# Kernel tuning notes

Measured on AMD Instinct MI355X. Metric: run time of the kernel, lower is better.

The kernel has to match this reference:

```python
import jax, jax.numpy as jnp
import numpy as np

FEAT = 1152
HID = [768, 512, 256]
WS = 32
LN_EPS = 1e-5


def _ln(x, g, b):
    mu = jnp.mean(x, axis=-1, keepdims=True)
    var = jnp.mean(jnp.square(x - mu), axis=-1, keepdims=True)
    return (x - mu) * jax.lax.rsqrt(var + LN_EPS) * g + b


def setup_inputs() -> dict:
    key = jax.random.key(0)
    ks = jax.random.split(key, 16)
    B, N, C = 8, 9216, FEAT

    def lin(k, din, dout):
        s = 1.0 / np.sqrt(din)
        k1, k2 = jax.random.split(k)
        return (jax.random.uniform(k1, (din, dout), jnp.float32, -s, s),
                jax.random.uniform(k2, (dout,), jnp.float32, -s, s))

    x = jax.random.normal(ks[0], (B, N, C), jnp.float32)
    W1, b1 = lin(ks[1], C, HID[0])
    W2, b2 = lin(ks[2], HID[0], HID[1])
    W3, b3 = lin(ks[3], HID[1], HID[2])
    Wo, bo = lin(ks[4], HID[2], C)
    red = C // 8
    ca_w1, ca_b1 = lin(ks[5], C, red)
    ca_w2, ca_b2 = lin(ks[6], red, C)
    return {
        "x": x,
        "W1": W1, "b1": b1, "g1": jnp.ones((HID[0],)), "be1": jnp.zeros((HID[0],)),
        "W2": W2, "b2": b2, "g2": jnp.ones((HID[1],)), "be2": jnp.zeros((HID[1],)),
        "W3": W3, "b3": b3, "g3": jnp.ones((HID[2],)), "be3": jnp.zeros((HID[2],)),
        "Wo": Wo, "bo": bo,
        "ca_w1": ca_w1, "ca_b1": ca_b1, "ca_w2": ca_w2, "ca_b2": ca_b2,
    }


def reference(x, W1, b1, g1, be1, W2, b2, g2, be2, W3, b3, g3, be3,
              Wo, bo, ca_w1, ca_b1, ca_w2, ca_b2):
    B, N, C = x.shape
    # projection + hidden blocks: Linear -> GELU(exact) -> LayerNorm
    h = _ln(jax.nn.gelu(x @ W1 + b1, approximate=False), g1, be1)
    h = _ln(jax.nn.gelu(h @ W2 + b2, approximate=False), g2, be2)
    h = _ln(jax.nn.gelu(h @ W3 + b3, approximate=False), g3, be3)
    y = h @ Wo + bo  # (B, N, C)
    # SE channel attention: global avg-pool over seq, 1x1 convs (=linear)
    pooled = jnp.mean(y, axis=1)                                  # (B, C)
    s = jax.nn.relu(pooled @ ca_w1 + ca_b1)                       # (B, C/8)
    s = jax.nn.sigmoid(s @ ca_w2 + ca_b2)                         # (B, C)
    y = y * s[:, None, :]
    # block-diagonal local self-attention, window = WS, scale 1/sqrt(C)
    nw = N // WS
    yw = y.reshape(B, nw, WS, C)
    scores = jnp.einsum('bwqc,bwkc->bwqk', yw, yw) / jnp.sqrt(jnp.asarray(C, y.dtype))
    attn = jax.nn.softmax(scores, axis=-1)
    out = jnp.einsum('bwqk,bwkc->bwqc', attn, yw)
    return out.reshape(B, N, C)
```

## Files before the change

kernel.cpp:

```cpp
#include <hip/hip_runtime.h>
#include <cstdint>
#include <cstddef>

typedef __bf16 bf16;
typedef __bf16 bf16x8 __attribute__((ext_vector_type(8)));
typedef float f32x4 __attribute__((ext_vector_type(4)));

__device__ __forceinline__ void gload_lds16(const bf16* g, bf16* l) {
    __builtin_amdgcn_global_load_lds((const __attribute__((address_space(1))) void*)g,
                                     (__attribute__((address_space(3))) void*)l, 16, 0, 0);
}

__global__ void wtrans_kernel(const float* __restrict__ W, bf16* __restrict__ Wt, int K, int N) {
    __shared__ bf16 tile[64][65];
    const int t = threadIdx.x;
    const int k0 = blockIdx.x << 6;
    const int n0 = blockIdx.y << 6;
#pragma unroll
    for (int i = 0; i < 16; ++i) {
        const int flat = i * 256 + t;
        const int r = flat >> 6;
        const int c = flat & 63;
        tile[c][r] = (bf16)W[(size_t)(k0 + r) * N + n0 + c];
    }
    __syncthreads();
#pragma unroll
    for (int i = 0; i < 16; ++i) {
        const int flat = i * 256 + t;
        const int r = flat >> 6;
        const int c = flat & 63;
        Wt[(size_t)(n0 + r) * K + k0 + c] = tile[r][c];
    }
}

__device__ __forceinline__ int xcd_swz(int bid, int nwg) {
    return (bid & 7) * (nwg >> 3) + (bid >> 3);
}

__global__ void gemm_bf16_kernel(const bf16* __restrict__ A, const bf16* __restrict__ Bt,
                                 const float* __restrict__ bias, bf16* __restrict__ C,
                                 int K, int N, int nx, int do_gelu)
{
    __shared__ bf16 Alds[128 * 64];
    __shared__ bf16 Blds[128 * 64];
    const int t = threadIdx.x;
    const int w = t >> 6;
    const int l = t & 63;
    const int l15 = l & 15, l4 = l >> 4;
    const int wgid = xcd_swz(blockIdx.x, gridDim.x);
    const int mblk = wgid / nx;
    const int nblk = wgid - mblk * nx;
    const int m0 = mblk << 7;
    const int n0 = nblk << 7;
    const int wm = (w >> 1) << 6;
    const int wn = (w & 1) << 6;

    f32x4 acc[4][4] = {};

    int sr[4], sg[4];
#pragma unroll
    for (int i = 0; i < 4; ++i) {
        const int flat = i * 256 + t;
        sr[i] = flat >> 3;
        sg[i] = ((flat & 7) ^ (sr[i] & 7)) << 3;
    }

    for (int k0 = 0; k0 < K; k0 += 64) {
#pragma unroll
        for (int i = 0; i < 4; ++i) {
            gload_lds16(A + (size_t)(m0 + sr[i]) * K + (k0 + sg[i]),
                        &Alds[(size_t)(i * 256 + (w << 6)) << 3]);
            gload_lds16(Bt + (size_t)(n0 + sr[i]) * K + (k0 + sg[i]),
                        &Blds[(size_t)(i * 256 + (w << 6)) << 3]);
        }
        __syncthreads();
#pragma unroll
        for (int kk = 0; kk < 2; ++kk) {
            bf16x8 af[4], bfv[4];
#pragma unroll
            for (int i = 0; i < 4; ++i) {
                const int r = wm + (i << 4) + l15;
                const int g = (kk << 2) + l4;
                af[i] = *(const bf16x8*)&Alds[(r << 6) + ((g ^ (r & 7)) << 3)];
                const int rn = wn + (i << 4) + l15;
                bfv[i] = *(const bf16x8*)&Blds[(rn << 6) + ((g ^ (rn & 7)) << 3)];
            }
#pragma unroll
            for (int i = 0; i < 4; ++i)
#pragma unroll
                for (int j = 0; j < 4; ++j)
                    acc[i][j] = __builtin_amdgcn_mfma_f32_16x16x32_bf16(af[i], bfv[j], acc[i][j], 0, 0, 0);
        }
        __syncthreads();
    }

#pragma unroll
    for (int i = 0; i < 4; ++i) {
        const int mb = m0 + wm + (i << 4) + (l4 << 2);
#pragma unroll
        for (int j = 0; j < 4; ++j) {
            const int col = n0 + wn + (j << 4) + l15;
            const float bv = bias[col];
#pragma unroll
            for (int r = 0; r < 4; ++r) {
                float v = acc[i][j][r] + bv;
                if (do_gelu) v = 0.5f * v * (1.0f + erff(v * 0.70710678118654752f));
                C[(size_t)(mb + r) * N + col] = (bf16)v;
            }
        }
    }
}

__global__ __launch_bounds__(256, 4)
void gemm_f32a_kernel(const float* __restrict__ A, const bf16* __restrict__ Bt,
                      const float* __restrict__ bias, bf16* __restrict__ C,
                      int K, int N, int nx)
{
    __shared__ bf16 Alds[128 * 64];
    __shared__ bf16 Blds[128 * 64];
    const int t = threadIdx.x;
    const int w = t >> 6;
    const int l = t & 63;
    const int l15 = l & 15, l4 = l >> 4;
    const int wgid = xcd_swz(blockIdx.x, gridDim.x);
    const int mblk = wgid / nx;
    const int nblk = wgid - mblk * nx;
    const int m0 = mblk << 7;
    const int n0 = nblk << 7;
    const int wm = (w >> 1) << 6;
    const int wn = (w & 1) << 6;

    f32x4 acc[4][4] = {};

    int arow[4], agrp[4];
#pragma unroll
    for (int i = 0; i < 4; ++i) {
        const int flat = i * 256 + t;
        arow[i] = flat >> 3;
        agrp[i] = flat & 7;
    }
    int br[4], bg[4];
#pragma unroll
    for (int i = 0; i < 4; ++i) {
        const int flat = i * 256 + t;
        br[i] = flat >> 3;
        bg[i] = ((flat & 7) ^ (br[i] & 7)) << 3;
    }

    for (int k0 = 0; k0 < K; k0 += 64) {
        float4 av0[4], av1[4];
#pragma unroll
        for (int i = 0; i < 4; ++i) {
            const float* src = A + (size_t)(m0 + arow[i]) * K + k0 + (agrp[i] << 3);
            av0[i] = *(const float4*)src;
            av1[i] = *(const float4*)(src + 4);
        }
#pragma unroll
        for (int i = 0; i < 4; ++i)
            gload_lds16(Bt + (size_t)(n0 + br[i]) * K + (k0 + bg[i]),
                        &Blds[(size_t)(i * 256 + (w << 6)) << 3]);
#pragma unroll
        for (int i = 0; i < 4; ++i) {
            bf16x8 o;
            o[0] = (bf16)av0[i].x; o[1] = (bf16)av0[i].y; o[2] = (bf16)av0[i].z; o[3] = (bf16)av0[i].w;
            o[4] = (bf16)av1[i].x; o[5] = (bf16)av1[i].y; o[6] = (bf16)av1[i].z; o[7] = (bf16)av1[i].w;
            *(bf16x8*)&Alds[(arow[i] << 6) + ((agrp[i] ^ (arow[i] & 7)) << 3)] = o;
        }
        __syncthreads();
#pragma unroll
        for (int kk = 0; kk < 2; ++kk) {
            bf16x8 af[4], bfv[4];
#pragma unroll
            for (int i = 0; i < 4; ++i) {
                const int r = wm + (i << 4) + l15;
                const int g = (kk << 2) + l4;
                af[i] = *(const bf16x8*)&Alds[(r << 6) + ((g ^ (r & 7)) << 3)];
                const int rn = wn + (i << 4) + l15;
                bfv[i] = *(const bf16x8*)&Blds[(rn << 6) + ((g ^ (rn & 7)) << 3)];
            }
#pragma unroll
            for (int i = 0; i < 4; ++i)
#pragma unroll
                for (int j = 0; j < 4; ++j)
                    acc[i][j] = __builtin_amdgcn_mfma_f32_16x16x32_bf16(af[i], bfv[j], acc[i][j], 0, 0, 0);
        }
        __syncthreads();
    }

#pragma unroll
    for (int i = 0; i < 4; ++i) {
        const int mb = m0 + wm + (i << 4) + (l4 << 2);
#pragma unroll
        for (int j = 0; j < 4; ++j) {
            const int col = n0 + wn + (j << 4) + l15;
            const float bv = bias[col];
#pragma unroll
            for (int r = 0; r < 4; ++r) {
                float v = acc[i][j][r] + bv;
                v = 0.5f * v * (1.0f + erff(v * 0.70710678118654752f));
                C[(size_t)(mb + r) * N + col] = (bf16)v;
            }
        }
    }
}

__global__ void ln768_kernel(bf16* __restrict__ H, const float* __restrict__ g,
                             const float* __restrict__ be)
{
    const int t = threadIdx.x;
    const int rloc = t >> 7;
    const int u = t & 127;
    bf16* hp = H + ((size_t)blockIdx.x * 2 + rloc) * 768;
    float v[8];
    float s1 = 0.f, s2 = 0.f;
    if (u < 96) {
        const bf16x8 hv = *(const bf16x8*)(hp + u * 8);
#pragma unroll
        for (int e = 0; e < 8; ++e) { v[e] = (float)hv[e]; s1 += v[e]; s2 += v[e] * v[e]; }
    }
#pragma unroll
    for (int m = 1; m < 64; m <<= 1) { s1 += __shfl_xor(s1, m, 64); s2 += __shfl_xor(s2, m, 64); }
    __shared__ float red[8];
    const int w = t >> 6;
    if ((t & 63) == 0) { red[w] = s1; red[w + 4] = s2; }
    __syncthreads();
    const int wb = rloc << 1;
    s1 = red[wb] + red[wb + 1];
    s2 = red[wb + 4] + red[wb + 5];
    const float mu = s1 * (1.0f / 768.0f);
    const float rstd = rsqrtf(s2 * (1.0f / 768.0f) - mu * mu + 1e-5f);
    if (u < 96) {
        const float4 g0 = *(const float4*)(g + u * 8);
        const float4 g1 = *(const float4*)(g + u * 8 + 4);
        const float4 b0 = *(const float4*)(be + u * 8);
        const float4 b1 = *(const float4*)(be + u * 8 + 4);
        bf16x8 o;
        o[0] = (bf16)((v[0] - mu) * rstd * g0.x + b0.x);
        o[1] = (bf16)((v[1] - mu) * rstd * g0.y + b0.y);
        o[2] = (bf16)((v[2] - mu) * rstd * g0.z + b0.z);
        o[3] = (bf16)((v[3] - mu) * rstd * g0.w + b0.w);
        o[4] = (bf16)((v[4] - mu) * rstd * g1.x + b1.x);
        o[5] = (bf16)((v[5] - mu) * rstd * g1.y + b1.y);
        o[6] = (bf16)((v[6] - mu) * rstd * g1.z + b1.z);
        o[7] = (bf16)((v[7] - mu) * rstd * g1.w + b1.w);
        *(bf16x8*)(hp + u * 8) = o;
    }
}

__global__ void ln512_kernel(bf16* __restrict__ H, const float* __restrict__ g,
                             const float* __restrict__ be)
{
    const int t = threadIdx.x;
    const int w = t >> 6, l = t & 63;
    bf16* hp = H + ((size_t)blockIdx.x * 4 + w) * 512;
    const bf16x8 hv = *(const bf16x8*)(hp + l * 8);
    float v[8];
    float s1 = 0.f, s2 = 0.f;
#pragma unroll
    for (int e = 0; e < 8; ++e) { v[e] = (float)hv[e]; s1 += v[e]; s2 += v[e] * v[e]; }
#pragma unroll
    for (int m = 1; m < 64; m <<= 1) { s1 += __shfl_xor(s1, m, 64); s2 += __shfl_xor(s2, m, 64); }
    const float mu = s1 * (1.0f / 512.0f);
    const float rstd = rsqrtf(s2 * (1.0f / 512.0f) - mu * mu + 1e-5f);
    const float4 g0 = *(const float4*)(g + l * 8);
    const float4 g1 = *(const float4*)(g + l * 8 + 4);
    const float4 b0 = *(const float4*)(be + l * 8);
    const float4 b1 = *(const float4*)(be + l * 8 + 4);
    bf16x8 o;
    o[0] = (bf16)((v[0] - mu) * rstd * g0.x + b0.x);
    o[1] = (bf16)((v[1] - mu) * rstd * g0.y + b0.y);
    o[2] = (bf16)((v[2] - mu) * rstd * g0.z + b0.z);
    o[3] = (bf16)((v[3] - mu) * rstd * g0.w + b0.w);
    o[4] = (bf16)((v[4] - mu) * rstd * g1.x + b1.x);
    o[5] = (bf16)((v[5] - mu) * rstd * g1.y + b1.y);
    o[6] = (bf16)((v[6] - mu) * rstd * g1.z + b1.z);
    o[7] = (bf16)((v[7] - mu) * rstd * g1.w + b1.w);
    *(bf16x8*)(hp + l * 8) = o;
}

__global__ void ln256_kernel(bf16* __restrict__ H, const float* __restrict__ g,
                             const float* __restrict__ be)
{
    const int t = threadIdx.x;
    const int rloc = t >> 5, l = t & 31;
    bf16* hp = H + ((size_t)blockIdx.x * 8 + rloc) * 256;
    const bf16x8 hv = *(const bf16x8*)(hp + l * 8);
    float v[8];
    float s1 = 0.f, s2 = 0.f;
#pragma unroll
    for (int e = 0; e < 8; ++e) { v[e] = (float)hv[e]; s1 += v[e]; s2 += v[e] * v[e]; }
#pragma unroll
    for (int m = 1; m < 32; m <<= 1) { s1 += __shfl_xor(s1, m, 64); s2 += __shfl_xor(s2, m, 64); }
    const float mu = s1 * (1.0f / 256.0f);
    const float rstd = rsqrtf(s2 * (1.0f / 256.0f) - mu * mu + 1e-5f);
    const float4 g0 = *(const float4*)(g + l * 8);
    const float4 g1 = *(const float4*)(g + l * 8 + 4);
    const float4 b0 = *(const float4*)(be + l * 8);
    const float4 b1 = *(const float4*)(be + l * 8 + 4);
    bf16x8 o;
    o[0] = (bf16)((v[0] - mu) * rstd * g0.x + b0.x);
    o[1] = (bf16)((v[1] - mu) * rstd * g0.y + b0.y);
    o[2] = (bf16)((v[2] - mu) * rstd * g0.z + b0.z);
    o[3] = (bf16)((v[3] - mu) * rstd * g0.w + b0.w);
    o[4] = (bf16)((v[4] - mu) * rstd * g1.x + b1.x);
    o[5] = (bf16)((v[5] - mu) * rstd * g1.y + b1.y);
    o[6] = (bf16)((v[6] - mu) * rstd * g1.z + b1.z);
    o[7] = (bf16)((v[7] - mu) * rstd * g1.w + b1.w);
    *(bf16x8*)(hp + l * 8) = o;
}

__global__ void pool1_kernel(const bf16* __restrict__ Y, float* __restrict__ ppart) {
    const int c = blockIdx.x * 128 + threadIdx.x;
    const int nc = blockIdx.y;
    const int b = blockIdx.z;
    const bf16* yp = Y + ((size_t)b * 9216 + (size_t)nc * 256) * 1152 + c;
    float s = 0.f;
#pragma unroll 4
    for (int i = 0; i < 256; ++i) s += (float)yp[(size_t)i * 1152];
    ppart[((size_t)b * 36 + nc) * 1152 + c] = s;
}

__global__ void pool2_kernel(const float* __restrict__ ppart, float* __restrict__ pooled) {
    const int i = blockIdx.x * 256 + threadIdx.x;
    const int b = i / 1152, c = i - b * 1152;
    float s = 0.f;
#pragma unroll
    for (int j = 0; j < 36; ++j) s += ppart[((size_t)b * 36 + j) * 1152 + c];
    pooled[i] = s;
}

__global__ void se_kernel(const float* __restrict__ pooled,
                          const float* __restrict__ w1, const float* __restrict__ b1,
                          const float* __restrict__ w2, const float* __restrict__ b2,
                          float* __restrict__ sbuf)
{
    const int b = blockIdx.x, t = threadIdx.x;
    __shared__ float p[1152];
    __shared__ float t1[144];
    for (int c = t; c < 1152; c += 256) p[c] = pooled[b * 1152 + c] * (1.0f / 9216.0f);
    __syncthreads();
    if (t < 144) {
        float a = b1[t];
        for (int k = 0; k < 1152; ++k) a += p[k] * w1[k * 144 + t];
        t1[t] = a > 0.f ? a : 0.f;
    }
    __syncthreads();
    for (int c = t; c < 1152; c += 256) {
        float a = b2[c];
#pragma unroll 8
        for (int k = 0; k < 144; ++k) a += t1[k] * w2[k * 1152 + c];
        sbuf[b * 1152 + c] = 1.0f / (1.0f + expf(-a));
    }
}

__global__ void attn_kernel(const bf16* __restrict__ Y, const float* __restrict__ sbuf,
                            float* __restrict__ out)
{
    __shared__ bf16 yw[32 * 384];
    __shared__ float Sp[4][32][33];
    __shared__ bf16 P[32 * 32];

    const int t = threadIdx.x;
    const int w = t >> 6, l = t & 63;
    const int l15 = l & 15, l4 = l >> 4;
    const int wdx = blockIdx.x, b = blockIdx.y;

    const bf16* Yp = Y + ((size_t)b * 9216 + (size_t)wdx * 32) * 1152;
    const float* sv = sbuf + b * 1152;
    float* op = out + ((size_t)b * 9216 + (size_t)wdx * 32) * 1152;

    auto stage_chunk = [&](int cc) {
#pragma unroll
        for (int i = 0; i < 6; ++i) {
            const int flat = i * 256 + t;
            const int r = flat / 48;
            const int gg = flat - r * 48;
            const int c0 = cc * 384 + gg * 8;
            const bf16x8 yv = *(const bf16x8*)(Yp + (size_t)r * 1152 + c0);
            const float4 sa = *(const float4*)(sv + c0);
            const float4 sb = *(const float4*)(sv + c0 + 4);
            bf16x8 ov;
            ov[0] = (bf16)((float)yv[0] * sa.x);
            ov[1] = (bf16)((float)yv[1] * sa.y);
            ov[2] = (bf16)((float)yv[2] * sa.z);
            ov[3] = (bf16)((float)yv[3] * sa.w);
            ov[4] = (bf16)((float)yv[4] * sb.x);
            ov[5] = (bf16)((float)yv[5] * sb.y);
            ov[6] = (bf16)((float)yv[6] * sb.z);
            ov[7] = (bf16)((float)yv[7] * sb.w);
            *(bf16x8*)&yw[((r * 48) + (gg ^ (r & 7))) << 3] = ov;
        }
    };

    f32x4 acc[2][2] = {};
    for (int cc = 0; cc < 3; ++cc) {
        if (cc) __syncthreads();
        stage_chunk(cc);
        __syncthreads();
#pragma unroll
        for (int kkl = 0; kkl < 3; ++kkl) {
            const int g = ((w * 3 + kkl) << 2) + l4;
            bf16x8 af[2];
#pragma unroll
            for (int i = 0; i < 2; ++i) {
                const int r = (i << 4) + l15;
                af[i] = *(const bf16x8*)&yw[((r * 48) + (g ^ (r & 7))) << 3];
            }
#pragma unroll
            for (int i = 0; i < 2; ++i)
#pragma unroll
                for (int j = 0; j < 2; ++j)
                    acc[i][j] = __builtin_amdgcn_mfma_f32_16x16x32_bf16(af[i], af[j], acc[i][j], 0, 0, 0);
        }
    }
#pragma unroll
    for (int i = 0; i < 2; ++i)
#pragma unroll
        for (int j = 0; j < 2; ++j)
#pragma unroll
            for (int r = 0; r < 4; ++r)
                Sp[w][(i << 4) + (l4 << 2) + r][(j << 4) + l15] = acc[i][j][r];
    __syncthreads();

    {
        const int q = t >> 3, u = t & 7;
        float v[4];
#pragma unroll
        for (int e = 0; e < 4; ++e) {
            const int k2 = (u << 2) + e;
            v[e] = (Sp[0][q][k2] + Sp[1][q][k2] + Sp[2][q][k2] + Sp[3][q][k2]) * 0.029462782549439483f;
        }
        float mx = fmaxf(fmaxf(v[0], v[1]), fmaxf(v[2], v[3]));
#pragma unroll
        for (int m = 1; m < 8; m <<= 1) mx = fmaxf(mx, __shfl_xor(mx, m, 64));
        float sm = 0.f;
#pragma unroll
        for (int e = 0; e < 4; ++e) { v[e] = expf(v[e] - mx); sm += v[e]; }
#pragma unroll
        for (int m = 1; m < 8; m <<= 1) sm += __shfl_xor(sm, m, 64);
        const float inv = 1.0f / sm;
#pragma unroll
        for (int e = 0; e < 4; ++e) P[(q << 5) + (u << 2) + e] = (bf16)(v[e] * inv);
    }
    __syncthreads();

    bf16x8 pa[2];
#pragma unroll
    for (int i = 0; i < 2; ++i)
        pa[i] = *(const bf16x8*)&P[(((i << 4) + l15) << 5) + (l4 << 3)];

    for (int ci = 0; ci < 3; ++ci) {
        const int cc = (ci == 0) ? 2 : (ci - 1);
        if (ci) {
            __syncthreads();
            stage_chunk(cc);
            __syncthreads();
        }
        f32x4 pacc[2][6] = {};
#pragma unroll
        for (int jn = 0; jn < 6; ++jn) {
            const int nl = w * 96 + (jn << 4) + l15;
            const int gg = nl >> 3, e = nl & 7;
            bf16x8 bv;
#pragma unroll
            for (int j = 0; j < 8; ++j) {
                const int kr = (l4 << 3) + j;
                bv[j] = yw[(((kr * 48) + (gg ^ (kr & 7))) << 3) + e];
            }
#pragma unroll
            for (int i = 0; i < 2; ++i)
                pacc[i][jn] = __builtin_amdgcn_mfma_f32_16x16x32_bf16(pa[i], bv, pacc[i][jn], 0, 0, 0);
        }
#pragma unroll
        for (int i = 0; i < 2; ++i) {
            const int mb = (i << 4) + (l4 << 2);
#pragma unroll
            for (int jn = 0; jn < 6; ++jn) {
                const int cg = cc * 384 + w * 96 + (jn << 4) + l15;
#pragma unroll
                for (int r = 0; r < 4; ++r)
                    op[(size_t)(mb + r) * 1152 + cg] = pacc[i][jn][r];
            }
        }
    }
}

extern "C" void kernel_launch(void* const* d_in, const int* in_sizes, int n_in,
                              void* d_out, int out_size, void* d_ws, size_t ws_size,
                              hipStream_t stream)
{
    const float* x   = (const float*)d_in[0];
    const float* W1  = (const float*)d_in[1];
    const float* b1  = (const float*)d_in[2];
    const float* g1  = (const float*)d_in[3];
    const float* be1 = (const float*)d_in[4];
    const float* W2  = (const float*)d_in[5];
    const float* b2  = (const float*)d_in[6];
    const float* g2  = (const float*)d_in[7];
    const float* be2 = (const float*)d_in[8];
    const float* W3  = (const float*)d_in[9];
    const float* b3  = (const float*)d_in[10];
    const float* g3  = (const float*)d_in[11];
    const float* be3 = (const float*)d_in[12];
    const float* Wo  = (const float*)d_in[13];
    const float* bo  = (const float*)d_in[14];
    const float* cw1 = (const float*)d_in[15];
    const float* cb1 = (const float*)d_in[16];
    const float* cw2 = (const float*)d_in[17];
    const float* cb2 = (const float*)d_in[18];
    float* out = (float*)d_out;

    const int M = 8 * 9216;
    size_t off = 0;
    auto alloc = [&](size_t nbytes) {
        void* p = (char*)d_ws + off;
        off += (nbytes + 255) & ~(size_t)255;
        return p;
    };
    bf16* Yb  = (bf16*)alloc((size_t)M * 1152 * 2);
    bf16* Hb  = (bf16*)alloc((size_t)M * 768 * 2);
    bf16* H2  = (bf16*)alloc((size_t)M * 512 * 2);
    bf16* Wt1 = (bf16*)alloc(768ull * 1152 * 2);
    bf16* Wt2 = (bf16*)alloc(512ull * 768 * 2);
    bf16* Wt3 = (bf16*)alloc(256ull * 512 * 2);
    bf16* Wto = (bf16*)alloc(1152ull * 256 * 2);
    float* ppart  = (float*)alloc(8ull * 36 * 1152 * 4);
    float* pooled = (float*)alloc(8ull * 1152 * 4);
    float* sbuf   = (float*)alloc(8ull * 1152 * 4);
    bf16* H1 = Hb;
    bf16* H3 = Hb;

    wtrans_kernel<<<dim3(18, 12), 256, 0, stream>>>(W1, Wt1, 1152, 768);
    wtrans_kernel<<<dim3(12, 8),  256, 0, stream>>>(W2, Wt2, 768, 512);
    wtrans_kernel<<<dim3(8, 4),   256, 0, stream>>>(W3, Wt3, 512, 256);
    wtrans_kernel<<<dim3(4, 18),  256, 0, stream>>>(Wo, Wto, 256, 1152);

    gemm_f32a_kernel<<<6 * 576, 256, 0, stream>>>(x, Wt1, b1, H1, 1152, 768, 6);
    ln768_kernel<<<M / 2, 256, 0, stream>>>(H1, g1, be1);
    gemm_bf16_kernel<<<4 * 576, 256, 0, stream>>>(H1, Wt2, b2, H2, 768, 512, 4, 1);
    ln512_kernel<<<M / 4, 256, 0, stream>>>(H2, g2, be2);
    gemm_bf16_kernel<<<2 * 576, 256, 0, stream>>>(H2, Wt3, b3, H3, 512, 256, 2, 1);
    ln256_kernel<<<M / 8, 256, 0, stream>>>(H3, g3, be3);
    gemm_bf16_kernel<<<9 * 576, 256, 0, stream>>>(H3, Wto, bo, Yb, 256, 1152, 9, 0);

    pool1_kernel<<<dim3(9, 36, 8), 128, 0, stream>>>(Yb, ppart);
    pool2_kernel<<<36, 256, 0, stream>>>(ppart, pooled);
    se_kernel<<<8, 256, 0, stream>>>(pooled, cw1, cb1, cw2, cb2, sbuf);
    attn_kernel<<<dim3(288, 8), 256, 0, stream>>>(Yb, sbuf, out);
}
```

Before: 891.8 us.

## Pre-convert input to bf16, merge weight transposes, fold pool2 into SE, reswizzle attn LDS

Replaces the fp32-A first GEMM with a separate elementwise fp32-to-bf16 conversion of x, after which the generic bf16 GEMM with async LDS loads handles layer one. The four weight-transpose launches become one kernel, and the pool2 reduction is folded into the SE kernel to save launches. The attention LDS swizzle now mixes higher row bits to reduce bank conflicts. The conversion adds a full extra read and write pass over x in exchange for a simpler, faster GEMM main loop.

After: 871.6 us. 1.02x faster.

```diff
diff --git a/kernel.cpp b/kernel.cpp
--- a/kernel.cpp
+++ b/kernel.cpp
@@ -11,11 +11,32 @@
                                      (__attribute__((address_space(3))) void*)l, 16, 0, 0);
 }
 
-__global__ void wtrans_kernel(const float* __restrict__ W, bf16* __restrict__ Wt, int K, int N) {
+__global__ void cvt_f32_bf16_kernel(const float* __restrict__ in, bf16* __restrict__ outp, size_t n) {
+    const size_t i = ((size_t)blockIdx.x * 256 + threadIdx.x) * 8;
+    if (i >= n) return;
+    const float4 a = *(const float4*)(in + i);
+    const float4 b = *(const float4*)(in + i + 4);
+    bf16x8 o;
+    o[0] = (bf16)a.x; o[1] = (bf16)a.y; o[2] = (bf16)a.z; o[3] = (bf16)a.w;
+    o[4] = (bf16)b.x; o[5] = (bf16)b.y; o[6] = (bf16)b.z; o[7] = (bf16)b.w;
+    *(bf16x8*)(outp + i) = o;
+}
+
+__global__ void wtrans_all_kernel(const float* __restrict__ W1, bf16* __restrict__ T1,
+                                  const float* __restrict__ W2, bf16* __restrict__ T2,
+                                  const float* __restrict__ W3, bf16* __restrict__ T3,
+                                  const float* __restrict__ Wo, bf16* __restrict__ To)
+{
     __shared__ bf16 tile[64][65];
-    const int t = threadIdx.x;
-    const int k0 = blockIdx.x << 6;
-    const int n0 = blockIdx.y << 6;
+    const int id = blockIdx.x;
+    const int t = threadIdx.x;
+    const float* W; bf16* T; int K, N, kb, nb;
+    if (id < 216)      { W = W1; T = T1; K = 1152; N = 768;  const int r = id;       kb = r % 18; nb = r / 18; }
+    else if (id < 312) { W = W2; T = T2; K = 768;  N = 512;  const int r = id - 216; kb = r % 12; nb = r / 12; }
+    else if (id < 344) { W = W3; T = T3; K = 512;  N = 256;  const int r = id - 312; kb = r % 8;  nb = r / 8;  }
+    else               { W = Wo; T = To; K = 256;  N = 1152; const int r = id - 344; kb = r % 4;  nb = r / 4;  }
+    const int k0 = kb << 6;
+    const int n0 = nb << 6;
 #pragma unroll
     for (int i = 0; i < 16; ++i) {
         const int flat = i * 256 + t;
@@ -29,7 +50,7 @@
         const int flat = i * 256 + t;
         const int r = flat >> 6;
         const int c = flat & 63;
-        Wt[(size_t)(n0 + r) * K + k0 + c] = tile[r][c];
+        T[(size_t)(n0 + r) * K + k0 + c] = tile[r][c];
     }
 }
 
@@ -105,99 +126,6 @@
             for (int r = 0; r < 4; ++r) {
                 float v = acc[i][j][r] + bv;
                 if (do_gelu) v = 0.5f * v * (1.0f + erff(v * 0.70710678118654752f));
-                C[(size_t)(mb + r) * N + col] = (bf16)v;
-            }
-        }
-    }
-}
-
-__global__ __launch_bounds__(256, 4)
-void gemm_f32a_kernel(const float* __restrict__ A, const bf16* __restrict__ Bt,
-                      const float* __restrict__ bias, bf16* __restrict__ C,
-                      int K, int N, int nx)
-{
-    __shared__ bf16 Alds[128 * 64];
-    __shared__ bf16 Blds[128 * 64];
-    const int t = threadIdx.x;
-    const int w = t >> 6;
-    const int l = t & 63;
-    const int l15 = l & 15, l4 = l >> 4;
-    const int wgid = xcd_swz(blockIdx.x, gridDim.x);
-    const int mblk = wgid / nx;
-    const int nblk = wgid - mblk * nx;
-    const int m0 = mblk << 7;
-    const int n0 = nblk << 7;
-    const int wm = (w >> 1) << 6;
-    const int wn = (w & 1) << 6;
-
-    f32x4 acc[4][4] = {};
-
-    int arow[4], agrp[4];
-#pragma unroll
-    for (int i = 0; i < 4; ++i) {
-        const int flat = i * 256 + t;
-        arow[i] = flat >> 3;
-        agrp[i] = flat & 7;
-    }
-    int br[4], bg[4];
-#pragma unroll
-    for (int i = 0; i < 4; ++i) {
-        const int flat = i * 256 + t;
-        br[i] = flat >> 3;
-        bg[i] = ((flat & 7) ^ (br[i] & 7)) << 3;
-    }
-
-    for (int k0 = 0; k0 < K; k0 += 64) {
-        float4 av0[4], av1[4];
-#pragma unroll
-        for (int i = 0; i < 4; ++i) {
-            const float* src = A + (size_t)(m0 + arow[i]) * K + k0 + (agrp[i] << 3);
-            av0[i] = *(const float4*)src;
-            av1[i] = *(const float4*)(src + 4);
-        }
-#pragma unroll
-        for (int i = 0; i < 4; ++i)
-            gload_lds16(Bt + (size_t)(n0 + br[i]) * K + (k0 + bg[i]),
-                        &Blds[(size_t)(i * 256 + (w << 6)) << 3]);
-#pragma unroll
-        for (int i = 0; i < 4; ++i) {
-            bf16x8 o;
-            o[0] = (bf16)av0[i].x; o[1] = (bf16)av0[i].y; o[2] = (bf16)av0[i].z; o[3] = (bf16)av0[i].w;
-            o[4] = (bf16)av1[i].x; o[5] = (bf16)av1[i].y; o[6] = (bf16)av1[i].z; o[7] = (bf16)av1[i].w;
-            *(bf16x8*)&Alds[(arow[i] << 6) + ((agrp[i] ^ (arow[i] & 7)) << 3)] = o;
-        }
-        __syncthreads();
-#pragma unroll
-        for (int kk = 0; kk < 2; ++kk) {
-            bf16x8 af[4], bfv[4];
-#pragma unroll
-            for (int i = 0; i < 4; ++i) {
-                const int r = wm + (i << 4) + l15;
-                const int g = (kk << 2) + l4;
-                af[i] = *(const bf16x8*)&Alds[(r << 6) + ((g ^ (r & 7)) << 3)];
-                const int rn = wn + (i << 4) + l15;
-                bfv[i] = *(const bf16x8*)&Blds[(rn << 6) + ((g ^ (rn & 7)) << 3)];
-            }
-#pragma unroll
-            for (int i = 0; i < 4; ++i)
-#pragma unroll
-                for (int j = 0; j < 4; ++j)
-                    acc[i][j] = __builtin_amdgcn_mfma_f32_16x16x32_bf16(af[i], bfv[j], acc[i][j], 0, 0, 0);
-        }
-        __syncthreads();
-    }
-
-#pragma unroll
-    for (int i = 0; i < 4; ++i) {
-        const int mb = m0 + wm + (i << 4) + (l4 << 2);
-#pragma unroll
-        for (int j = 0; j < 4; ++j) {
-            const int col = n0 + wn + (j << 4) + l15;
-            const float bv = bias[col];
-#pragma unroll
-            for (int r = 0; r < 4; ++r) {
-                float v = acc[i][j][r] + bv;
-                v = 0.5f * v * (1.0f + erff(v * 0.70710678118654752f));
                 C[(size_t)(mb + r) * N + col] = (bf16)v;
             }
         }
@@ -320,16 +248,7 @@
     ppart[((size_t)b * 36 + nc) * 1152 + c] = s;
 }
 
-__global__ void pool2_kernel(const float* __restrict__ ppart, float* __restrict__ pooled) {
-    const int i = blockIdx.x * 256 + threadIdx.x;
-    const int b = i / 1152, c = i - b * 1152;
-    float s = 0.f;
-#pragma unroll
-    for (int j = 0; j < 36; ++j) s += ppart[((size_t)b * 36 + j) * 1152 + c];
-    pooled[i] = s;
-}
-
-__global__ void se_kernel(const float* __restrict__ pooled,
+__global__ void se_kernel(const float* __restrict__ ppart,
                           const float* __restrict__ w1, const float* __restrict__ b1,
                           const float* __restrict__ w2, const float* __restrict__ b2,
                           float* __restrict__ sbuf)
@@ -337,7 +256,12 @@
     const int b = blockIdx.x, t = threadIdx.x;
     __shared__ float p[1152];
     __shared__ float t1[144];
-    for (int c = t; c < 1152; c += 256) p[c] = pooled[b * 1152 + c] * (1.0f / 9216.0f);
+    for (int c = t; c < 1152; c += 256) {
+        float s = 0.f;
+#pragma unroll
+        for (int j = 0; j < 36; ++j) s += ppart[((size_t)b * 36 + j) * 1152 + c];
+        p[c] = s * (1.0f / 9216.0f);
+    }
     __syncthreads();
     if (t < 144) {
         float a = b1[t];
@@ -352,6 +276,8 @@
         sbuf[b * 1152 + c] = 1.0f / (1.0f + expf(-a));
     }
 }
+
+__device__ __forceinline__ int fswz(int r) { return (r & 7) ^ ((r >> 3) & 3); }
 
 __global__ void attn_kernel(const bf16* __restrict__ Y, const float* __restrict__ sbuf,
                             float* __restrict__ out)
@@ -388,7 +314,7 @@
             ov[5] = (bf16)((float)yv[5] * sb.y);
             ov[6] = (bf16)((float)yv[6] * sb.z);
             ov[7] = (bf16)((float)yv[7] * sb.w);
-            *(bf16x8*)&yw[((r * 48) + (gg ^ (r & 7))) << 3] = ov;
+            *(bf16x8*)&yw[((r * 48) + (gg ^ fswz(r))) << 3] = ov;
         }
     };
 
@@ -404,7 +330,7 @@
 #pragma unroll
             for (int i = 0; i < 2; ++i) {
                 const int r = (i << 4) + l15;
-                af[i] = *(const bf16x8*)&yw[((r * 48) + (g ^ (r & 7))) << 3];
+                af[i] = *(const bf16x8*)&yw[((r * 48) + (g ^ fswz(r))) << 3];
             }
 #pragma unroll
             for (int i = 0; i < 2; ++i)
@@ -465,7 +391,7 @@
 #pragma unroll
             for (int j = 0; j < 8; ++j) {
                 const int kr = (l4 << 3) + j;
-                bv[j] = yw[(((kr * 48) + (gg ^ (kr & 7))) << 3) + e];
+                bv[j] = yw[(((kr * 48) + (gg ^ fswz(kr))) << 3) + e];
             }
 #pragma unroll
             for (int i = 0; i < 2; ++i)
@@ -524,18 +450,16 @@
     bf16* Wt2 = (bf16*)alloc(512ull * 768 * 2);
     bf16* Wt3 = (bf16*)alloc(256ull * 512 * 2);
     bf16* Wto = (bf16*)alloc(1152ull * 256 * 2);
-    float* ppart  = (float*)alloc(8ull * 36 * 1152 * 4);
-    float* pooled = (float*)alloc(8ull * 1152 * 4);
-    float* sbuf   = (float*)alloc(8ull * 1152 * 4);
+    float* ppart = (float*)alloc(8ull * 36 * 1152 * 4);
+    float* sbuf  = (float*)alloc(8ull * 1152 * 4);
+    bf16* Xb = Yb;
     bf16* H1 = Hb;
     bf16* H3 = Hb;
 
-    wtrans_kernel<<<dim3(18, 12), 256, 0, stream>>>(W1, Wt1, 1152, 768);
-    wtrans_kernel<<<dim3(12, 8),  256, 0, stream>>>(W2, Wt2, 768, 512);
-    wtrans_kernel<<<dim3(8, 4),   256, 0, stream>>>(W3, Wt3, 512, 256);
-    wtrans_kernel<<<dim3(4, 18),  256, 0, stream>>>(Wo, Wto, 256, 1152);
-
-    gemm_f32a_kernel<<<6 * 576, 256, 0, stream>>>(x, Wt1, b1, H1, 1152, 768, 6);
+    cvt_f32_bf16_kernel<<<41472, 256, 0, stream>>>(x, Xb, (size_t)M * 1152);
+    wtrans_all_kernel<<<416, 256, 0, stream>>>(W1, Wt1, W2, Wt2, W3, Wt3, Wo, Wto);
+
+    gemm_bf16_kernel<<<6 * 576, 256, 0, stream>>>(Xb, Wt1, b1, H1, 1152, 768, 6, 1);
     ln768_kernel<<<M / 2, 256, 0, stream>>>(H1, g1, be1);
     gemm_bf16_kernel<<<4 * 576, 256, 0, stream>>>(H1, Wt2, b2, H2, 768, 512, 4, 1);
     ln512_kernel<<<M / 4, 256, 0, stream>>>(H2, g2, be2);
@@ -544,7 +468,6 @@
     gemm_bf16_kernel<<<9 * 576, 256, 0, stream>>>(H3, Wto, bo, Yb, 256, 1152, 9, 0);
 
     pool1_kernel<<<dim3(9, 36, 8), 128, 0, stream>>>(Yb, ppart);
-    pool2_kernel<<<36, 256, 0, stream>>>(ppart, pooled);
-    se_kernel<<<8, 256, 0, stream>>>(pooled, cw1, cb1, cw2, cb2, sbuf);
+    se_kernel<<<8, 256, 0, stream>>>(ppart, cw1, cb1, cw2, cb2, sbuf);
     attn_kernel<<<dim3(288, 8), 256, 0, stream>>>(Yb, sbuf, out);
 }
```
